# Kernel tuning notes

Hardware: AMD Instinct MI355X
Metric: run time of the kernel (lower is better)

## Reference

```python
import jax, jax.numpy as jnp
import numpy as np

P, H_OUT, D, NX = 32, 1, 256, 16
S_A = -0.1

def layernorm(x, g, b, eps=1e-5):
    mu = jnp.mean(x, axis=-1, keepdims=True)
    var = jnp.var(x, axis=-1, keepdims=True)
    return (x - mu) * jax.lax.rsqrt(var + eps) * g + b

def setup_inputs() -> dict:
    key = jax.random.key(0)
    ks = jax.random.split(key, 16)
    B, L = 8, 2048
    y = jax.random.normal(ks[0], (B, L, P), jnp.float32)
    Win = jax.random.normal(ks[1], (P, D), jnp.float32) / np.sqrt(P)
    bin_ = jnp.zeros((D,), jnp.float32)
    ng = jnp.ones((D,), jnp.float32); nb = jnp.zeros((D,), jnp.float32)
    # A = -10*rand + s_A, with A[:,0] = s_A (fix first state of each channel)
    A = -10.0 * jax.random.uniform(ks[2], (D, NX), jnp.float32) + S_A
    A = A.at[:, 0].set(S_A)
    W_B = jax.random.normal(ks[3], (NX, D), jnp.float32)
    W_C = jax.random.normal(ks[4], (NX, D), jnp.float32)
    q_delta = jax.random.normal(ks[5], (D,), jnp.float32)
    p_delta = jax.random.normal(ks[6], (1,), jnp.float32)
    nfg = jnp.ones((D,), jnp.float32); nfb = jnp.zeros((D,), jnp.float32)
    W1 = jax.random.normal(ks[7], (D, D), jnp.float32) / np.sqrt(D)
    b1 = jnp.zeros((D,), jnp.float32)
    W2 = jax.random.normal(ks[8], (D, H_OUT * P), jnp.float32) / np.sqrt(D)
    b2 = jnp.zeros((H_OUT * P,), jnp.float32)
    return {"y": y, "Win": Win, "bin_": bin_, "ng": ng, "nb": nb, "A": A,
            "W_B": W_B, "W_C": W_C, "q_delta": q_delta, "p_delta": p_delta,
            "nfg": nfg, "nfb": nfb, "W1": W1, "b1": b1, "W2": W2, "b2": b2}

def selective_scan(u, delta, A, Bm, Cm):
    # u: (B,L,D), delta: (B,L), A: (D,NX), Bm/Cm: (B,L,NX)
    dA = jnp.exp(delta[..., None, None] * A)                      # (B,L,D,NX)
    dBu = delta[..., None, None] * Bm[:, :, None, :] * u[..., None]  # (B,L,D,NX)
    x0 = jnp.zeros((u.shape[0], u.shape[2], A.shape[1]), u.dtype)
    def step(x, inp):
        dA_t, dBu_t, C_t = inp
        x = dA_t * x + dBu_t                                      # (B,D,NX)
        y_t = jnp.einsum('bdn,bn->bd', x, C_t)
        return x, y_t
    _, ys = jax.lax.scan(step, x0, (dA.transpose(1, 0, 2, 3),
                                    dBu.transpose(1, 0, 2, 3),
                                    Cm.transpose(1, 0, 2)))
    return ys.transpose(1, 0, 2)                                  # (B,L,D)

def reference(y, Win, bin_, ng, nb, A, W_B, W_C, q_delta, p_delta,
              nfg, nfb, W1, b1, W2, b2):
    B, L, _ = y.shape
    h = y @ Win + bin_                                            # (B,L,D)
    hn = layernorm(h, ng, nb)
    delta = jax.nn.softplus(p_delta[0] + jnp.einsum('bld,d->bl', hn, q_delta))
    Bm = jnp.einsum('nd,bld->bln', W_B, hn)
    Cm = jnp.einsum('nd,bld->bln', W_C, hn)
    upd = selective_scan(hn, delta, A, Bm, Cm)
    h = h + upd
    h = layernorm(h, nfg, nfb)
    out = jax.nn.gelu(h @ W1 + b1, approximate=False) @ W2 + b2
    return out.reshape(B, L, H_OUT, P)
```

## Files before the change

### kernel.cpp

```cpp
#include <hip/hip_runtime.h>
#include <math.h>

#define D 256
#define NX 16
#define L 2048
#define NBATCH 8
#define NTOK (NBATCH * L)
#define CL 32
#define NCH (L / CL)
#define LOG2E 1.44269504088896340736f

typedef float f32x4 __attribute__((ext_vector_type(4)));
typedef short bf16x8 __attribute__((ext_vector_type(8)));

__device__ __forceinline__ unsigned short f2bf(float x) {
  unsigned u = __float_as_uint(x);
  u = u + 0x7fffu + ((u >> 16) & 1u);
  return (unsigned short)(u >> 16);
}
__device__ __forceinline__ float bf2f(unsigned short h) {
  return __uint_as_float(((unsigned)h) << 16);
}

__global__ __launch_bounds__(256) void k0_prep(const float* __restrict__ A,
                                               const float* __restrict__ WB,
                                               const float* __restrict__ WC,
                                               const float* __restrict__ W1,
                                               const float* __restrict__ W2,
                                               float* __restrict__ At,
                                               float* __restrict__ Wbct,
                                               unsigned short* __restrict__ W1fh,
                                               unsigned short* __restrict__ W1fl,
                                               unsigned short* __restrict__ W2fh,
                                               unsigned short* __restrict__ W2fl) {
  int i = blockIdx.x * 256 + threadIdx.x;
  if (i < 4096) {
    int d = i >> 4, n = i & 15;
    At[n * D + d] = A[i] * LOG2E;
  } else if (i < 12288) {
    int j = i - 4096;
    int d = j >> 5, c = j & 31;
    Wbct[j] = (c < 16) ? WB[c * D + d] : WC[(c - 16) * D + d];
  } else if (i < 77824) {
    int e = i - 12288;
    int j = e & 7, l = (e >> 3) & 63, tt = (e >> 9) & 15, s = e >> 13;
    int k = s * 32 + ((l >> 4) << 3) + j;
    int n = tt * 16 + (l & 15);
    float x = W1[k * 256 + n];
    unsigned short h = f2bf(x);
    W1fh[e] = h;
    W1fl[e] = f2bf(x - bf2f(h));
  } else {
    int e = i - 77824;
    int j = e & 7, l = (e >> 3) & 63, tt = (e >> 9) & 1, s = e >> 10;
    int k = s * 32 + ((l >> 4) << 3) + j;
    int n = tt * 16 + (l & 15);
    float x = W2[k * 32 + n];
    unsigned short h = f2bf(x);
    W2fh[e] = h;
    W2fl[e] = f2bf(x - bf2f(h));
  }
}

__global__ __launch_bounds__(256, 4) void k1a_front_scan(
    const float* __restrict__ y, const float* __restrict__ Win,
    const float* __restrict__ bin_, const float* __restrict__ ng,
    const float* __restrict__ nb, const float* __restrict__ Wbct,
    const float* __restrict__ qd, const float* __restrict__ pd,
    const float* __restrict__ At,
    float* __restrict__ hn, float* __restrict__ delta,
    float* __restrict__ Bm, float* __restrict__ Cm,
    float* __restrict__ muv, float* __restrict__ irsv,
    float* __restrict__ EX, float* __restrict__ T) {
  __shared__ float sy[32][32];
  __shared__ float sh[32][260];
  __shared__ float sB[32][NX];
  __shared__ float sdelta[32];
  int t = threadIdx.x;
  int tok0 = blockIdx.x * 32;
  {
    const float4* src = (const float4*)(y + (size_t)tok0 * 32);
    ((float4*)sy)[t] = src[t];
  }
  __syncthreads();
  int dcol = t & 63;
  int jrow = t >> 6;
  int d4 = dcol * 4;
  float4 bv = ((const float4*)bin_)[dcol];
  float4 g4 = ((const float4*)ng)[dcol];
  float4 nb4 = ((const float4*)nb)[dcol];
  float4 q4 = ((const float4*)qd)[dcol];
  float pd0 = pd[0];
  const float4* Win4 = (const float4*)Win;
  for (int g = 0; g < 4; ++g) {
    int j0 = jrow * 8 + g * 2;
    float4 acc0 = bv, acc1 = bv;
    #pragma unroll 4
    for (int k = 0; k < 32; ++k) {
      float4 wv = Win4[k * 64 + dcol];
      float a0 = sy[j0][k];
      float a1 = sy[j0 + 1][k];
      acc0.x = fmaf(a0, wv.x, acc0.x); acc1.x = fmaf(a1, wv.x, acc1.x);
      acc0.y = fmaf(a0, wv.y, acc0.y); acc1.y = fmaf(a1, wv.y, acc1.y);
      acc0.z = fmaf(a0, wv.z, acc0.z); acc1.z = fmaf(a1, wv.z, acc1.z);
      acc0.w = fmaf(a0, wv.w, acc0.w); acc1.w = fmaf(a1, wv.w, acc1.w);
    }
    #pragma unroll
    for (int p = 0; p < 2; ++p) {
      int j = j0 + p;
      int tok = tok0 + j;
      float4 a = (p == 0) ? acc0 : acc1;
      float s1 = a.x + a.y + a.z + a.w;
      float s2 = a.x * a.x + a.y * a.y + a.z * a.z + a.w * a.w;
      #pragma unroll
      for (int off = 1; off < 64; off <<= 1) {
        s1 += __shfl_xor(s1, off);
        s2 += __shfl_xor(s2, off);
      }
      float mu = s1 * (1.f / D);
      float var = s2 * (1.f / D) - mu * mu;
      float rstd = rsqrtf(var + 1e-5f);
      if (dcol == 0) { muv[tok] = mu; irsv[tok] = sqrtf(var + 1e-5f); }
      float4 v4;
      v4.x = (a.x - mu) * rstd * g4.x + nb4.x;
      v4.y = (a.y - mu) * rstd * g4.y + nb4.y;
      v4.z = (a.z - mu) * rstd * g4.z + nb4.z;
      v4.w = (a.w - mu) * rstd * g4.w + nb4.w;
      ((float4*)(hn + (size_t)tok * D))[dcol] = v4;
      *(float4*)&sh[j][d4] = v4;
      float dd = v4.x * q4.x + v4.y * q4.y + v4.z * q4.z + v4.w * q4.w;
      #pragma unroll
      for (int off = 1; off < 64; off <<= 1) dd += __shfl_xor(dd, off);
      if (dcol == 0) {
        float xx = pd0 + dd;
        float dv = (xx > 20.f) ? xx : log1pf(expf(xx));
        delta[tok] = dv;
        sdelta[j] = dv;
      }
    }
  }
  __syncthreads();
  if (t < 32) {
    float v = sdelta[t];
    #pragma unroll
    for (int off = 1; off < 32; off <<= 1) v += __shfl_xor(v, off);
    if (t == 0) T[blockIdx.x] = v;
  }
  int col4 = t & 7;
  int j = t >> 3;
  const float4* W4 = (const float4*)Wbct;
  float4 o = make_float4(0.f, 0.f, 0.f, 0.f);
  #pragma unroll 4
  for (int d = 0; d < 256; ++d) {
    float av = sh[j][d];
    float4 w = W4[d * 8 + col4];
    o.x = fmaf(av, w.x, o.x);
    o.y = fmaf(av, w.y, o.y);
    o.z = fmaf(av, w.z, o.z);
    o.w = fmaf(av, w.w, o.w);
  }
  int tokj = tok0 + j;
  if (col4 < 4) {
    ((float4*)(Bm + (size_t)tokj * NX))[col4] = o;
    *(float4*)&sB[j][col4 * 4] = o;
  } else {
    ((float4*)(Cm + (size_t)tokj * NX))[col4 - 4] = o;
  }
  __syncthreads();
  float a16[16];
  #pragma unroll
  for (int n = 0; n < 16; ++n) a16[n] = At[n * D + t];
  float x16[16];
  #pragma unroll
  for (int n = 0; n < 16; ++n) x16[n] = 0.f;
  for (int lo = 0; lo < CL; ++lo) {
    float dlt = sdelta[lo];
    float du = dlt * sh[lo][t];
    #pragma unroll
    for (int n = 0; n < 16; ++n)
      x16[n] = fmaf(exp2f(dlt * a16[n]), x16[n], du * sB[lo][n]);
  }
  size_t exbase = (size_t)blockIdx.x * (NX * D) + t;
  #pragma unroll
  for (int n = 0; n < 16; ++n) EX[exbase + n * D] = x16[n];
}

__global__ __launch_bounds__(64) void k2b_chunkscan(
    const float* __restrict__ At, const float* __restrict__ T,
    float* __restrict__ EX) {
  __shared__ float sT[NCH];
  int b = blockIdx.x >> 6;
  int rem = ((blockIdx.x & 63) << 6) | threadIdx.x;
  sT[threadIdx.x] = T[b * NCH + threadIdx.x];
  __syncthreads();
  float A2 = At[rem];
  size_t base = ((size_t)b << 18) + rem;
  float eq[4];
  #pragma unroll
  for (int j = 0; j < 4; ++j) eq[j] = EX[base + ((size_t)j << 12)];
  float x = 0.f;
  #pragma unroll 4
  for (int c = 0; c < NCH; ++c) {
    float e = eq[c & 3];
    if (c + 4 < NCH) eq[c & 3] = EX[base + ((size_t)(c + 4) << 12)];
    EX[base + ((size_t)c << 12)] = x;
    x = fmaf(exp2f(sT[c] * A2), x, e);
  }
}

__device__ __forceinline__ float gelu_exact(float x) {
  return 0.5f * x * (1.f + erff(x * 0.70710678118654752440f));
}

__global__ __launch_bounds__(256) void k2cd_scan_mlp(
    const float* __restrict__ hn, const float* __restrict__ delta,
    const float* __restrict__ Bm, const float* __restrict__ Cm,
    const float* __restrict__ At, const float* __restrict__ EX,
    const float* __restrict__ muv, const float* __restrict__ irsv,
    const float* __restrict__ ng, const float* __restrict__ nb,
    const float* __restrict__ nfg, const float* __restrict__ nfb,
    const unsigned short* __restrict__ W1fh, const unsigned short* __restrict__ W1fl,
    const unsigned short* __restrict__ W2fh, const unsigned short* __restrict__ W2fl,
    const float* __restrict__ b1, const float* __restrict__ b2,
    float* __restrict__ out) {
  __shared__ float s_az[32 * 260];
  __shared__ __align__(16) unsigned short sAh[32 * 256];
  __shared__ __align__(16) unsigned short sAl[32 * 256];
  __shared__ float sB[32][NX];
  __shared__ float sC[32][NX];
  __shared__ float sdelta[32];
  __shared__ float smu[32];
  __shared__ float sirs[32];
  int t = threadIdx.x;
  int tok0 = blockIdx.x * 32;
  size_t tokbase = (size_t)tok0;
  if (t < 32) {
    sdelta[t] = delta[tokbase + t];
    smu[t] = muv[tokbase + t];
    sirs[t] = irsv[tokbase + t];
  }
  for (int i = t; i < 32 * NX; i += 256) {
    ((float*)sB)[i] = Bm[tokbase * NX + i];
    ((float*)sC)[i] = Cm[tokbase * NX + i];
  }
  float a16[16], x16[16];
  size_t exbase = (size_t)blockIdx.x * (NX * D) + t;
  #pragma unroll
  for (int n = 0; n < 16; ++n) {
    a16[n] = At[n * D + t];
    x16[n] = EX[exbase + n * D];
  }
  float nb_d = nb[t];
  float invg = 1.0f / ng[t];
  __syncthreads();
  for (int lo = 0; lo < CL; ++lo) {
    float hv = hn[(tokbase + lo) * D + t];
    float dlt = sdelta[lo];
    float du = dlt * hv;
    float p = 0.f;
    #pragma unroll
    for (int n = 0; n < 16; ++n) {
      x16[n] = fmaf(exp2f(dlt * a16[n]), x16[n], du * sB[lo][n]);
      p = fmaf(x16[n], sC[lo][n], p);
    }
    float h = fmaf((hv - nb_d) * invg, sirs[lo], smu[lo]);
    s_az[lo * 260 + t] = h + p;
  }
  __syncthreads();
  int dcol = t & 63, jrow = t >> 6;
  int d4 = dcol * 4, j8 = jrow * 8;
  {
    float4 g4 = ((const float4*)nfg)[dcol];
    float4 b4 = ((const float4*)nfb)[dcol];
    for (int jj = 0; jj < 8; ++jj) {
      int lo = j8 + jj;
      float4 v = *(float4*)&s_az[lo * 260 + d4];
      float s1 = v.x + v.y + v.z + v.w;
      float s2 = v.x * v.x + v.y * v.y + v.z * v.z + v.w * v.w;
      #pragma unroll
      for (int off = 1; off < 64; off <<= 1) {
        s1 += __shfl_xor(s1, off);
        s2 += __shfl_xor(s2, off);
      }
      float mu2 = s1 * (1.f / D);
      float var2 = s2 * (1.f / D) - mu2 * mu2;
      float rstd2 = rsqrtf(var2 + 1e-5f);
      float4 o;
      o.x = (v.x - mu2) * rstd2 * g4.x + b4.x;
      o.y = (v.y - mu2) * rstd2 * g4.y + b4.y;
      o.z = (v.z - mu2) * rstd2 * g4.z + b4.z;
      o.w = (v.w - mu2) * rstd2 * g4.w + b4.w;
      unsigned short h0 = f2bf(o.x), h1 = f2bf(o.y), h2 = f2bf(o.z), h3 = f2bf(o.w);
      unsigned short q0 = f2bf(o.x - bf2f(h0));
      unsigned short q1 = f2bf(o.y - bf2f(h1));
      unsigned short q2 = f2bf(o.z - bf2f(h2));
      unsigned short q3 = f2bf(o.w - bf2f(h3));
      unsigned off16 = ((unsigned)(d4 * 2)) ^ ((unsigned)(lo & 7) << 4);
      uint2 hv2, lv2;
      hv2.x = (unsigned)h0 | ((unsigned)h1 << 16);
      hv2.y = (unsigned)h2 | ((unsigned)h3 << 16);
      lv2.x = (unsigned)q0 | ((unsigned)q1 << 16);
      lv2.y = (unsigned)q2 | ((unsigned)q3 << 16);
      *(uint2*)((char*)sAh + lo * 512 + off16) = hv2;
      *(uint2*)((char*)sAl + lo * 512 + off16) = lv2;
    }
  }
  __syncthreads();
  int l = t & 63, w = t >> 6;
  const bf16x8* B1h = (const bf16x8*)W1fh;
  const bf16x8* B1l = (const bf16x8*)W1fl;
  f32x4 acc[2][4];
  #pragma unroll
  for (int m = 0; m < 2; ++m)
    #pragma unroll
    for (int n = 0; n < 4; ++n) {
      f32x4 z4 = {0.f, 0.f, 0.f, 0.f};
      acc[m][n] = z4;
    }
  #pragma unroll 2
  for (int s = 0; s < 8; ++s) {
    bf16x8 ah[2], al[2];
    #pragma unroll
    for (int m = 0; m < 2; ++m) {
      int row = m * 16 + (l & 15);
      unsigned off16 = ((unsigned)(s * 64 + ((l >> 4) << 4))) ^ ((unsigned)(row & 7) << 4);
      ah[m] = *(const bf16x8*)((const char*)sAh + row * 512 + off16);
      al[m] = *(const bf16x8*)((const char*)sAl + row * 512 + off16);
    }
    #pragma unroll
    for (int n = 0; n < 4; ++n) {
      int bi = (s * 16 + w * 4 + n) * 64 + l;
      bf16x8 bh = B1h[bi];
      bf16x8 bl = B1l[bi];
      #pragma unroll
      for (int m = 0; m < 2; ++m) {
        acc[m][n] = __builtin_amdgcn_mfma_f32_16x16x32_bf16(ah[m], bh, acc[m][n], 0, 0, 0);
        acc[m][n] = __builtin_amdgcn_mfma_f32_16x16x32_bf16(al[m], bh, acc[m][n], 0, 0, 0);
        acc[m][n] = __builtin_amdgcn_mfma_f32_16x16x32_bf16(ah[m], bl, acc[m][n], 0, 0, 0);
        acc[m][n] = __builtin_amdgcn_mfma_f32_16x16x32_bf16(al[m], bl, acc[m][n], 0, 0, 0);
      }
    }
  }
  __syncthreads();
  #pragma unroll
  for (int n = 0; n < 4; ++n) {
    int colz = w * 64 + n * 16 + (l & 15);
    float b1v = b1[colz];
    #pragma unroll
    for (int m = 0; m < 2; ++m) {
      #pragma unroll
      for (int r = 0; r < 4; ++r) {
        int row = m * 16 + ((l >> 4) << 2) + r;
        float zv = gelu_exact(acc[m][n][r] + b1v);
        unsigned short zh = f2bf(zv);
        unsigned short zl = f2bf(zv - bf2f(zh));
        unsigned off16 = ((unsigned)(colz * 2)) ^ ((unsigned)(row & 7) << 4);
        *(unsigned short*)((char*)sAh + row * 512 + off16) = zh;
        *(unsigned short*)((char*)sAl + row * 512 + off16) = zl;
      }
    }
  }
  __syncthreads();
  int mw = w >> 1, nw = w & 1;
  const bf16x8* B2h = (const bf16x8*)W2fh;
  const bf16x8* B2l = (const bf16x8*)W2fl;
  f32x4 acc2 = {0.f, 0.f, 0.f, 0.f};
  #pragma unroll 2
  for (int s = 0; s < 8; ++s) {
    int row = mw * 16 + (l & 15);
    unsigned off16 = ((unsigned)(s * 64 + ((l >> 4) << 4))) ^ ((unsigned)(row & 7) << 4);
    bf16x8 zh8 = *(const bf16x8*)((const char*)sAh + row * 512 + off16);
    bf16x8 zl8 = *(const bf16x8*)((const char*)sAl + row * 512 + off16);
    int bi = (s * 2 + nw) * 64 + l;
    bf16x8 bh = B2h[bi];
    bf16x8 bl = B2l[bi];
    acc2 = __builtin_amdgcn_mfma_f32_16x16x32_bf16(zh8, bh, acc2, 0, 0, 0);
    acc2 = __builtin_amdgcn_mfma_f32_16x16x32_bf16(zl8, bh, acc2, 0, 0, 0);
    acc2 = __builtin_amdgcn_mfma_f32_16x16x32_bf16(zh8, bl, acc2, 0, 0, 0);
    acc2 = __builtin_amdgcn_mfma_f32_16x16x32_bf16(zl8, bl, acc2, 0, 0, 0);
  }
  int colo = nw * 16 + (l & 15);
  float b2v = b2[colo];
  #pragma unroll
  for (int r = 0; r < 4; ++r) {
    int row = mw * 16 + ((l >> 4) << 2) + r;
    out[(size_t)(tok0 + row) * 32 + colo] = acc2[r] + b2v;
  }
}

extern "C" void kernel_launch(void* const* d_in, const int* in_sizes, int n_in,
                              void* d_out, int out_size, void* d_ws, size_t ws_size,
                              hipStream_t stream) {
  const float* y    = (const float*)d_in[0];
  const float* Win  = (const float*)d_in[1];
  const float* bin_ = (const float*)d_in[2];
  const float* ng   = (const float*)d_in[3];
  const float* nb   = (const float*)d_in[4];
  const float* A    = (const float*)d_in[5];
  const float* WB   = (const float*)d_in[6];
  const float* WC   = (const float*)d_in[7];
  const float* qd   = (const float*)d_in[8];
  const float* pd   = (const float*)d_in[9];
  const float* nfg  = (const float*)d_in[10];
  const float* nfb  = (const float*)d_in[11];
  const float* W1   = (const float*)d_in[12];
  const float* b1   = (const float*)d_in[13];
  const float* W2   = (const float*)d_in[14];
  const float* b2   = (const float*)d_in[15];

  float* ws = (float*)d_ws;
  float* hnbuf = ws;
  float* delta = ws + 4194304;
  float* Bm    = delta + NTOK;
  float* Cm    = Bm + NTOK * NX;
  float* muv   = Cm + NTOK * NX;
  float* irsv  = muv + NTOK;
  float* Tbuf  = irsv + NTOK;
  float* At    = Tbuf + NBATCH * NCH;
  float* Wbct  = At + D * NX;
  float* EX    = Wbct + D * 32;
  unsigned short* W1fh = (unsigned short*)(EX + 2097152);
  unsigned short* W1fl = W1fh + 65536;
  unsigned short* W2fh = W1fl + 65536;
  unsigned short* W2fl = W2fh + 8192;

  k0_prep<<<336, 256, 0, stream>>>(A, WB, WC, W1, W2, At, Wbct,
                                   W1fh, W1fl, W2fh, W2fl);
  k1a_front_scan<<<NTOK / 32, 256, 0, stream>>>(y, Win, bin_, ng, nb, Wbct,
                                                qd, pd, At, hnbuf, delta, Bm,
                                                Cm, muv, irsv, EX, Tbuf);
  k2b_chunkscan<<<NBATCH * 64, 64, 0, stream>>>(At, Tbuf, EX);
  k2cd_scan_mlp<<<NTOK / 32, 256, 0, stream>>>(hnbuf, delta, Bm, Cm, At, EX,
                                               muv, irsv, ng, nb, nfg, nfb,
                                               W1fh, W1fl, W2fh, W2fl,
                                               b1, b2, (float*)d_out);
}
```

Before: 210.2 us.

## Double k1a thread count, split B/C projection K-dim and scan states across halves

```diff
diff --git a/kernel.cpp b/kernel.cpp
--- a/kernel.cpp
+++ b/kernel.cpp
@@ -62,7 +62,7 @@
   }
 }
 
-__global__ __launch_bounds__(256, 4) void k1a_front_scan(
+__global__ __launch_bounds__(512, 4) void k1a_front_scan(
     const float* __restrict__ y, const float* __restrict__ Win,
     const float* __restrict__ bin_, const float* __restrict__ ng,
     const float* __restrict__ nb, const float* __restrict__ Wbct,
@@ -76,9 +76,10 @@
   __shared__ float sh[32][260];
   __shared__ float sB[32][NX];
   __shared__ float sdelta[32];
+  __shared__ float sph[2 * 32 * 32];
   int t = threadIdx.x;
   int tok0 = blockIdx.x * 32;
-  {
+  if (t < 256) {
     const float4* src = (const float4*)(y + (size_t)tok0 * 32);
     ((float4*)sy)[t] = src[t];
   }
@@ -92,8 +93,8 @@
   float4 q4 = ((const float4*)qd)[dcol];
   float pd0 = pd[0];
   const float4* Win4 = (const float4*)Win;
-  for (int g = 0; g < 4; ++g) {
-    int j0 = jrow * 8 + g * 2;
+  for (int g = 0; g < 2; ++g) {
+    int j0 = jrow * 4 + g * 2;
     float4 acc0 = bv, acc1 = bv;
     #pragma unroll 4
     for (int k = 0; k < 32; ++k) {
@@ -146,43 +147,62 @@
     for (int off = 1; off < 32; off <<= 1) v += __shfl_xor(v, off);
     if (t == 0) T[blockIdx.x] = v;
   }
-  int col4 = t & 7;
-  int j = t >> 3;
-  const float4* W4 = (const float4*)Wbct;
-  float4 o = make_float4(0.f, 0.f, 0.f, 0.f);
-  #pragma unroll 4
-  for (int d = 0; d < 256; ++d) {
-    float av = sh[j][d];
-    float4 w = W4[d * 8 + col4];
-    o.x = fmaf(av, w.x, o.x);
-    o.y = fmaf(av, w.y, o.y);
-    o.z = fmaf(av, w.z, o.z);
-    o.w = fmaf(av, w.w, o.w);
-  }
-  int tokj = tok0 + j;
-  if (col4 < 4) {
-    ((float4*)(Bm + (size_t)tokj * NX))[col4] = o;
-    *(float4*)&sB[j][col4 * 4] = o;
-  } else {
-    ((float4*)(Cm + (size_t)tokj * NX))[col4 - 4] = o;
-  }
-  __syncthreads();
-  float a16[16];
-  #pragma unroll
-  for (int n = 0; n < 16; ++n) a16[n] = At[n * D + t];
-  float x16[16];
-  #pragma unroll
-  for (int n = 0; n < 16; ++n) x16[n] = 0.f;
-  for (int lo = 0; lo < CL; ++lo) {
-    float dlt = sdelta[lo];
-    float du = dlt * sh[lo][t];
-    #pragma unroll
-    for (int n = 0; n < 16; ++n)
-      x16[n] = fmaf(exp2f(dlt * a16[n]), x16[n], du * sB[lo][n]);
-  }
-  size_t exbase = (size_t)blockIdx.x * (NX * D) + t;
-  #pragma unroll
-  for (int n = 0; n < 16; ++n) EX[exbase + n * D] = x16[n];
+  {
+    int hk = t >> 8;
+    int r = t & 255;
+    int col4 = r & 7;
+    int j = r >> 3;
+    const float* shrow = &sh[j][hk * 128];
+    const float4* W4 = (const float4*)Wbct + (size_t)hk * 128 * 8;
+    float4 o = make_float4(0.f, 0.f, 0.f, 0.f);
+    #pragma unroll 4
+    for (int k = 0; k < 128; ++k) {
+      float av = shrow[k];
+      float4 wv = W4[k * 8 + col4];
+      o.x = fmaf(av, wv.x, o.x);
+      o.y = fmaf(av, wv.y, o.y);
+      o.z = fmaf(av, wv.z, o.z);
+      o.w = fmaf(av, wv.w, o.w);
+    }
+    *(float4*)&sph[((hk * 32 + j) << 5) + col4 * 4] = o;
+  }
+  __syncthreads();
+  if (t < 256) {
+    int j = t >> 3, cc = t & 7;
+    float4 r0 = *(float4*)&sph[(j << 5) + cc * 4];
+    float4 r1 = *(float4*)&sph[((32 + j) << 5) + cc * 4];
+    float4 r;
+    r.x = r0.x + r1.x; r.y = r0.y + r1.y;
+    r.z = r0.z + r1.z; r.w = r0.w + r1.w;
+    int tokj = tok0 + j;
+    if (cc < 4) {
+      ((float4*)(Bm + (size_t)tokj * NX))[cc] = r;
+      *(float4*)&sB[j][cc * 4] = r;
+    } else {
+      ((float4*)(Cm + (size_t)tokj * NX))[cc - 4] = r;
+    }
+  }
+  __syncthreads();
+  {
+    int half = t >> 8;
+    int d = t & 255;
+    float a8[8], x8[8];
+    #pragma unroll
+    for (int n = 0; n < 8; ++n) {
+      a8[n] = At[(half * 8 + n) * D + d];
+      x8[n] = 0.f;
+    }
+    for (int lo = 0; lo < CL; ++lo) {
+      float dlt = sdelta[lo];
+      float du = dlt * sh[lo][d];
+      #pragma unroll
+      for (int n = 0; n < 8; ++n)
+        x8[n] = fmaf(exp2f(dlt * a8[n]), x8[n], du * sB[lo][half * 8 + n]);
+    }
+    size_t exbase = (size_t)blockIdx.x * (NX * D) + d;
+    #pragma unroll
+    for (int n = 0; n < 8; ++n) EX[exbase + (half * 8 + n) * D] = x8[n];
+  }
 }
 
 __global__ __launch_bounds__(64) void k2b_chunkscan(
@@ -195,14 +215,14 @@
   __syncthreads();
   float A2 = At[rem];
   size_t base = ((size_t)b << 18) + rem;
-  float eq[4];
+  float eq[8];
   #pragma unroll
-  for (int j = 0; j < 4; ++j) eq[j] = EX[base + ((size_t)j << 12)];
+  for (int j = 0; j < 8; ++j) eq[j] = EX[base + ((size_t)j << 12)];
   float x = 0.f;
-  #pragma unroll 4
+  #pragma unroll 8
   for (int c = 0; c < NCH; ++c) {
-    float e = eq[c & 3];
-    if (c + 4 < NCH) eq[c & 3] = EX[base + ((size_t)(c + 4) << 12)];
+    float e = eq[c & 7];
+    if (c + 8 < NCH) eq[c & 7] = EX[base + ((size_t)(c + 8) << 12)];
     EX[base + ((size_t)c << 12)] = x;
     x = fmaf(exp2f(sT[c] * A2), x, e);
   }
@@ -426,7 +446,7 @@
 
   k0_prep<<<336, 256, 0, stream>>>(A, WB, WC, W1, W2, At, Wbct,
                                    W1fh, W1fl, W2fh, W2fl);
-  k1a_front_scan<<<NTOK / 32, 256, 0, stream>>>(y, Win, bin_, ng, nb, Wbct,
+  k1a_front_scan<<<NTOK / 32, 512, 0, stream>>>(y, Win, bin_, ng, nb, Wbct,
                                                 qd, pd, At, hnbuf, delta, Bm,
                                                 Cm, muv, irsv, EX, Tbuf);
   k2b_chunkscan<<<NBATCH * 64, 64, 0, stream>>>(At, Tbuf, EX);
```

Result: faster. 199.4 us (-5.1%).
